# Kernel tuning notes

Measured on AMD Instinct MI355X. Metric: run time of the kernel, lower is better.

## Reference

```python
import jax, jax.numpy as jnp
import numpy as np

VOCAB, E, H, P, B, S = 30522, 1024, 1024, 16, 32, 256
HD = H // 2  # per-direction LSTM hidden


def _lstm_dir(xt, Wih, Whh, bih, bhh, reverse):
    # xt: [S,B,in]; PyTorch gate order i,f,g,o
    Hd = Whh.shape[1]
    Bz = xt.shape[1]
    bias = bih + bhh

    def step(carry, xb):
        h, c = carry
        g = xb @ Wih.T + h @ Whh.T + bias
        i, f, gg, o = jnp.split(g, 4, axis=-1)
        c = jax.nn.sigmoid(f) * c + jax.nn.sigmoid(i) * jnp.tanh(gg)
        h = jax.nn.sigmoid(o) * jnp.tanh(c)
        return (h, c), h

    init = (jnp.zeros((Bz, Hd), xt.dtype), jnp.zeros((Bz, Hd), xt.dtype))
    _, hs = jax.lax.scan(step, init, xt, reverse=reverse)
    return hs  # [S,B,Hd], time-ordered


def _bilstm(x, Wih, Whh, bih, bhh):
    # x: [B,S,in]; Wih: [2,4*HD,in] (dir 0 = fwd, dir 1 = bwd)
    xt = jnp.swapaxes(x, 0, 1)
    fw = _lstm_dir(xt, Wih[0], Whh[0], bih[0], bhh[0], False)
    bw = _lstm_dir(xt, Wih[1], Whh[1], bih[1], bhh[1], True)
    return jnp.swapaxes(jnp.concatenate([fw, bw], axis=-1), 0, 1)  # [B,S,2*HD]


def setup_inputs() -> dict:
    key = jax.random.key(0)
    ks = jax.random.split(key, 20)
    sc = 0.05
    inp = {}
    inp["emb"] = jax.random.normal(ks[0], (VOCAB, E), jnp.float32) * sc
    inp["ctx_emb"] = jax.random.normal(ks[1], (VOCAB, E), jnp.float32) * sc
    inp["prompt_emb"] = jax.random.normal(ks[2], (P, E), jnp.float32) * sc
    # LSTM layer 0: input E; layer 1: input 2*HD = H
    inp["Wih0"] = jax.random.normal(ks[3], (2, 4 * HD, E), jnp.float32) * sc
    inp["Whh0"] = jax.random.normal(ks[4], (2, 4 * HD, HD), jnp.float32) * sc
    inp["bih0"] = jax.random.normal(ks[5], (2, 4 * HD), jnp.float32) * sc
    inp["bhh0"] = jax.random.normal(ks[6], (2, 4 * HD), jnp.float32) * sc
    inp["Wih1"] = jax.random.normal(ks[7], (2, 4 * HD, H), jnp.float32) * sc
    inp["Whh1"] = jax.random.normal(ks[8], (2, 4 * HD, HD), jnp.float32) * sc
    inp["bih1"] = jax.random.normal(ks[9], (2, 4 * HD), jnp.float32) * sc
    inp["bhh1"] = jax.random.normal(ks[10], (2, 4 * HD), jnp.float32) * sc
    inp["W1"] = jax.random.normal(ks[11], (H, H), jnp.float32) * sc
    inp["b1"] = jnp.zeros((H,), jnp.float32)
    inp["W2"] = jax.random.normal(ks[12], (E, H), jnp.float32) * sc
    inp["b2"] = jnp.zeros((E,), jnp.float32)
    inp["input_ids"] = jax.random.randint(ks[13], (B, S), 0, VOCAB)
    # distinct, sorted prompt positions per batch row (torch loop assumes valid slots)
    pk = jax.random.split(ks[14], B)
    perms = jax.vmap(lambda k: jax.random.permutation(k, S)[:P])(pk)
    inp["prompt_indexes"] = jnp.sort(perms, axis=1)
    return inp


def reference(emb, ctx_emb, prompt_emb, Wih0, Whh0, bih0, bhh0,
              Wih1, Whh1, bih1, bhh1, W1, b1, W2, b2,
              input_ids, prompt_indexes):
    raw = emb[input_ids]                               # [B,S,E]
    b_idx = jnp.arange(input_ids.shape[0])[:, None]    # [B,1]
    # unique_prompt branch: detached raw + ctx embedding, scatter prompt embeds
    allb = jax.lax.stop_gradient(raw) + ctx_emb[input_ids]
    allb = allb.at[b_idx, prompt_indexes].set(
        jnp.broadcast_to(prompt_emb, (input_ids.shape[0],) + prompt_emb.shape))
    h = _bilstm(allb, Wih0, Whh0, bih0, bhh0)
    h = _bilstm(h, Wih1, Whh1, bih1, bhh1)             # [B,S,H]
    out = jax.nn.relu(h @ W1.T + b1) @ W2.T + b2       # [B,S,E]
    upd = out[b_idx, prompt_indexes] + prompt_emb      # [B,P,E]
    return raw.at[b_idx, prompt_indexes].set(upd)
```

## Files before the change

kernel.cpp:

```cpp
#include <hip/hip_runtime.h>
#include <hip/hip_bf16.h>
#include <math.h>

constexpr int NB  = 32;
constexpr int NS  = 256;
constexpr int NE  = 1024;
constexpr int NH  = 1024;
constexpr int NHD = 512;
constexpr int NG  = 2048;
constexpr int NP  = 16;
constexpr int NBS = NB * NS;
constexpr int GK  = 1024;

constexpr int UPW  = 16;
constexpr int NWGD = NHD / UPW;
constexpr size_t GT_DIR = (size_t)NWGD * 256 * 2048;

typedef __attribute__((ext_vector_type(8))) short bf16x8;
typedef __attribute__((ext_vector_type(4))) float f32x4;
typedef unsigned short u16;

__device__ __forceinline__ float sigm(float x) { return 1.0f / (1.0f + __expf(-x)); }
__device__ __forceinline__ u16 f2bf(float f) {
    union { float f; unsigned u; } v; v.f = f;
    unsigned r = v.u + 0x7FFF + ((v.u >> 16) & 1);
    return (u16)(r >> 16);
}
__device__ __forceinline__ float bf2f(u16 b) {
    return __uint_as_float((unsigned)b << 16);
}

__global__ void k_zero(int* p) { p[threadIdx.x] = 0; }

__global__ void k_allb(const float* __restrict__ emb, const float* __restrict__ ctx,
                       const float* __restrict__ pemb, const int* __restrict__ ids,
                       const int* __restrict__ pidx, u16* __restrict__ allb) {
    int r = blockIdx.x;
    int b = r >> 8, s = r & 255;
    __shared__ int ppos;
    if (threadIdx.x == 0) {
        int t = -1;
        #pragma unroll
        for (int p = 0; p < NP; ++p)
            if (pidx[b * NP + p] == s) t = p;
        ppos = t;
    }
    __syncthreads();
    int e = threadIdx.x;
    float4 v;
    if (ppos >= 0) {
        v = ((const float4*)(pemb + (size_t)ppos * NE))[e];
    } else {
        int id = ids[r];
        float4 a = ((const float4*)(emb + (size_t)id * NE))[e];
        float4 c = ((const float4*)(ctx + (size_t)id * NE))[e];
        v = make_float4(a.x + c.x, a.y + c.y, a.z + c.z, a.w + c.w);
    }
    ushort4 o;
    o.x = f2bf(v.x); o.y = f2bf(v.y); o.z = f2bf(v.z); o.w = f2bf(v.w);
    *(ushort4*)(allb + ((size_t)(s * NB + b)) * NE + e * 4) = o;
}

__global__ void k_raw(const float* __restrict__ emb, const int* __restrict__ ids,
                      float* __restrict__ out) {
    int r = blockIdx.x;
    int id = ids[r];
    ((float4*)(out + (size_t)r * NE))[threadIdx.x] =
        ((const float4*)(emb + (size_t)id * NE))[threadIdx.x];
}

__global__ void k_wcvt(const float* __restrict__ Wih, const float* __restrict__ bih,
                       const float* __restrict__ bhh, u16* __restrict__ Wbf,
                       float* __restrict__ biasC) {
    int blk = blockIdx.x;
    int d = blk >> 11, np = blk & 2047;
    int rw = (np & 3) * 512 + (np >> 2);
    const float* src = Wih + ((size_t)d * NG + rw) * GK;
    u16* dst = Wbf + ((size_t)d * NG + np) * GK;
    int t = threadIdx.x;
    float4 v = ((const float4*)src)[t];
    ushort4 o;
    o.x = f2bf(v.x); o.y = f2bf(v.y); o.z = f2bf(v.z); o.w = f2bf(v.w);
    ((ushort4*)dst)[t] = o;
    if (t == 0)
        biasC[d * NG + np] = bih[d * NG + rw] + bhh[d * NG + rw];
}

__global__ __launch_bounds__(256) void k_gemm_m(const u16* __restrict__ A0,
                                                const u16* __restrict__ A1,
                                                int astride,
                                                const u16* __restrict__ W,
                                                const float* __restrict__ bc,
                                                float* __restrict__ Gt) {
    __shared__ char At[128 * 128];
    __shared__ char Wt[128 * 128];
    int tid = threadIdx.x;
    int lane = tid & 63, w = tid >> 6;
    int n0 = blockIdx.x * 128, m0 = blockIdx.y * 128;
    int r = tid >> 1, h = tid & 1;

    f32x4 acc[4][4];
    #pragma unroll
    for (int i = 0; i < 4; ++i)
        #pragma unroll
        for (int j = 0; j < 4; ++j) acc[i][j] = (f32x4){0.f, 0.f, 0.f, 0.f};

    unsigned rsw = (unsigned)((r & 7) << 4);
    for (int kt = 0; kt < GK; kt += 64) {
        {
            int k0 = kt + h * 32;
            const u16* asrc = (k0 < 512) ? (A0 + (size_t)(m0 + r) * astride + k0)
                                         : (A1 + (size_t)(m0 + r) * astride + (k0 - 512));
            const u16* wsrc = W + (size_t)(n0 + r) * GK + k0;
            #pragma unroll
            for (int j = 0; j < 4; ++j) {
                uint4 va = *(const uint4*)(asrc + j * 8);
                *(uint4*)(At + r * 128 + (((unsigned)(h * 64 + j * 16)) ^ rsw)) = va;
                uint4 vw = *(const uint4*)(wsrc + j * 8);
                *(uint4*)(Wt + r * 128 + (((unsigned)(h * 64 + j * 16)) ^ rsw)) = vw;
            }
        }
        __syncthreads();
        #pragma unroll
        for (int sub = 0; sub < 2; ++sub) {
            bf16x8 af[4], bfr[4];
            int kbyte = sub * 64 + (lane >> 4) * 16;
            #pragma unroll
            for (int ni = 0; ni < 4; ++ni) {
                int rr = (w & 1) * 64 + ni * 16 + (lane & 15);
                af[ni] = *(const bf16x8*)(Wt + rr * 128 + ((unsigned)kbyte ^ ((unsigned)((rr & 7) << 4))));
            }
            #pragma unroll
            for (int mi = 0; mi < 4; ++mi) {
                int rr = (w >> 1) * 64 + mi * 16 + (lane & 15);
                bfr[mi] = *(const bf16x8*)(At + rr * 128 + ((unsigned)kbyte ^ ((unsigned)((rr & 7) << 4))));
            }
            #pragma unroll
            for (int mi = 0; mi < 4; ++mi)
                #pragma unroll
                for (int ni = 0; ni < 4; ++ni)
                    acc[mi][ni] = __builtin_amdgcn_mfma_f32_16x16x32_bf16(
                        af[ni], bfr[mi], acc[mi][ni], 0, 0, 0);
        }
        __syncthreads();
    }
    #pragma unroll
    for (int mi = 0; mi < 4; ++mi) {
        int mp = m0 + (w >> 1) * 64 + mi * 16 + (lane & 15);
        int t = mp >> 5, b = mp & 31;
        #pragma unroll
        for (int ni = 0; ni < 4; ++ni) {
            int npb = n0 + (w & 1) * 64 + ni * 16 + (lane >> 4) * 4;
            int unit = npb >> 2;
            float4 bv = *(const float4*)(bc + npb);
            f32x4 a = acc[mi][ni];
            float4 o = make_float4(a[0] + bv.x, a[1] + bv.y, a[2] + bv.z, a[3] + bv.w);
            *(float4*)(Gt + ((size_t)((unit >> 4) * NS + t)) * 2048 + b * 64 + (unit & 15) * 4) = o;
        }
    }
}

__global__ __launch_bounds__(256) void k_lstm_s(const float* __restrict__ Gt,
                                                const float* __restrict__ Whh,
                                                u16* __restrict__ hxb,
                                                int* __restrict__ ctr) {
    __shared__ char hlds[NB * NHD * 2];
    int wg = blockIdx.x;
    int d = wg & 1;
    int slice = wg >> 1;
    int n0 = slice * UPW;
    int tid = threadIdx.x;
    int lane = tid & 63;
    int w = tid >> 6;
    int* ctrd  = ctr + d * 64;
    int* myctr = ctrd + (slice & 3) * 16;
    u16* hxd = hxb + (size_t)d * NS * NB * NHD;
    const float* Gd = Gt + (size_t)d * GT_DIR + (size_t)slice * NS * 2048;

    bf16x8 wfrag[16];
    {
        int rloc = lane & 15;
        int usub = rloc >> 2, g = rloc & 3;
        int kb = lane >> 4;
        const float* wrow = Whh + ((size_t)d * NG + g * NHD + n0 + 4 * w + usub) * NHD;
        #pragma unroll
        for (int kk = 0; kk < 16; ++kk) {
            const float* p = wrow + kk * 32 + kb * 8;
            float4 x = *(const float4*)p;
            float4 y = *(const float4*)(p + 4);
            bf16x8 wf;
            wf[0] = (short)f2bf(x.x); wf[1] = (short)f2bf(x.y);
            wf[2] = (short)f2bf(x.z); wf[3] = (short)f2bf(x.w);
            wf[4] = (short)f2bf(y.x); wf[5] = (short)f2bf(y.y);
            wf[6] = (short)f2bf(y.z); wf[7] = (short)f2bf(y.w);
            wfrag[kk] = wf;
        }
    }
    int uloc  = 4 * w + (lane >> 4);
    int unitC = n0 + uloc;
    int bcol0 = lane & 15;
    int bcol1 = 16 + bcol0;
    int kb    = lane >> 4;
    int c8 = tid & 7, bRow = tid >> 3;

    float c0 = 0.f, c1 = 0.f;
    int ttp = d ? (NS - 1) : 0;
    float4 Gv0 = *(const float4*)(Gd + (size_t)ttp * 2048 + bcol0 * 64 + uloc * 4);
    float4 Gv1 = *(const float4*)(Gd + (size_t)ttp * 2048 + bcol1 * 64 + uloc * 4);

    for (int step = 0; step < NS; ++step) {
        int tt = d ? (NS - 1 - step) : step;
        f32x4 acc0 = {0.f, 0.f, 0.f, 0.f};
        f32x4 acc1 = {0.f, 0.f, 0.f, 0.f};
        if (step) {
            int tprev = d ? tt + 1 : tt - 1;
            const u16* srow = hxd + ((size_t)tprev * NB + bRow) * NHD;
            char* dstrow = hlds + bRow * 1024;
            unsigned rsw = (unsigned)((bRow & 7) << 4);
            #pragma unroll
            for (int i = 0; i < 8; ++i) {
                uint4 v = *(const uint4*)(srow + c8 * 64 + i * 8);
                *(uint4*)(dstrow + (((unsigned)(c8 * 128 + i * 16)) ^ rsw)) = v;
            }
            __syncthreads();
            const char* b0base = hlds + bcol0 * 1024;
            const char* b1base = hlds + bcol1 * 1024;
            unsigned s0 = (unsigned)((bcol0 & 7) << 4);
            unsigned s1 = (unsigned)((bcol1 & 7) << 4);
            #pragma unroll
            for (int kk = 0; kk < 16; ++kk) {
                bf16x8 b0 = *(const bf16x8*)(b0base + (((unsigned)(kk * 64 + kb * 16)) ^ s0));
                bf16x8 b1 = *(const bf16x8*)(b1base + (((unsigned)(kk * 64 + kb * 16)) ^ s1));
                acc0 = __builtin_amdgcn_mfma_f32_16x16x32_bf16(wfrag[kk], b0, acc0, 0, 0, 0);
                acc1 = __builtin_amdgcn_mfma_f32_16x16x32_bf16(wfrag[kk], b1, acc1, 0, 0, 0);
            }
        }
        {
            float ig = sigm(acc0[0] + Gv0.x);
            float fg = sigm(acc0[1] + Gv0.y);
            float gg = tanhf(acc0[2] + Gv0.z);
            float og = sigm(acc0[3] + Gv0.w);
            c0 = fg * c0 + ig * gg;
            float hv = og * tanhf(c0);
            __hip_atomic_store(hxd + ((size_t)tt * NB + bcol0) * NHD + unitC, f2bf(hv),
                               __ATOMIC_RELAXED, __HIP_MEMORY_SCOPE_AGENT);
        }
        {
            float ig = sigm(acc1[0] + Gv1.x);
            float fg = sigm(acc1[1] + Gv1.y);
            float gg = tanhf(acc1[2] + Gv1.z);
            float og = sigm(acc1[3] + Gv1.w);
            c1 = fg * c1 + ig * gg;
            float hv = og * tanhf(c1);
            __hip_atomic_store(hxd + ((size_t)tt * NB + bcol1) * NHD + unitC, f2bf(hv),
                               __ATOMIC_RELAXED, __HIP_MEMORY_SCOPE_AGENT);
        }
        asm volatile("s_waitcnt vmcnt(0)" ::: "memory");
        __syncthreads();
        if (tid == 0)
            __hip_atomic_fetch_add(myctr, 1, __ATOMIC_RELAXED, __HIP_MEMORY_SCOPE_AGENT);
        if (step + 1 < NS) {
            int ttn = d ? tt - 1 : tt + 1;
            Gv0 = *(const float4*)(Gd + (size_t)ttn * 2048 + bcol0 * 64 + uloc * 4);
            Gv1 = *(const float4*)(Gd + (size_t)ttn * 2048 + bcol1 * 64 + uloc * 4);
        }
        asm volatile("" ::: "memory");
        if (tid == 0) {
            int target = (NWGD / 4) * (step + 1);
            for (;;) {
                int a = __hip_atomic_load(ctrd +  0, __ATOMIC_RELAXED, __HIP_MEMORY_SCOPE_AGENT);
                int b = __hip_atomic_load(ctrd + 16, __ATOMIC_RELAXED, __HIP_MEMORY_SCOPE_AGENT);
                int c = __hip_atomic_load(ctrd + 32, __ATOMIC_RELAXED, __HIP_MEMORY_SCOPE_AGENT);
                int e = __hip_atomic_load(ctrd + 48, __ATOMIC_RELAXED, __HIP_MEMORY_SCOPE_AGENT);
                if (a >= target && b >= target && c >= target && e >= target) break;
                __builtin_amdgcn_s_sleep(1);
            }
        }
        __syncthreads();
    }
}

__global__ __launch_bounds__(256) void k_mlp1(const u16* __restrict__ hxb,
                                              const int* __restrict__ pidx,
                                              const float* __restrict__ W1,
                                              const float* __restrict__ b1,
                                              float* __restrict__ mid) {
    __shared__ float As[16][65];
    __shared__ float Ws[16][65];
    int tid = threadIdx.x;
    int tx = tid & 15, ty = tid >> 4;
    int n0 = blockIdx.x * 64, m0 = blockIdx.y * 64;
    int lr = tid >> 2;
    int lk = (tid & 3) * 4;
    int m = m0 + lr;
    int bb = m >> 4;
    int s = pidx[m];
    float acc[4][4] = {};
    for (int kt = 0; kt < GK; kt += 16) {
        int k0 = kt + lk;
        int half = k0 >> 9;
        ushort4 av4 = *(const ushort4*)(hxb + (((size_t)(half * NS + s)) * NB + bb) * NHD + (k0 & 511));
        float4 wv = *(const float4*)(W1 + (size_t)(n0 + lr) * GK + k0);
        As[lk + 0][lr] = bf2f(av4.x); As[lk + 1][lr] = bf2f(av4.y);
        As[lk + 2][lr] = bf2f(av4.z); As[lk + 3][lr] = bf2f(av4.w);
        Ws[lk + 0][lr] = wv.x; Ws[lk + 1][lr] = wv.y;
        Ws[lk + 2][lr] = wv.z; Ws[lk + 3][lr] = wv.w;
        __syncthreads();
        #pragma unroll
        for (int kk = 0; kk < 16; ++kk) {
            float a[4], wv2[4];
            #pragma unroll
            for (int i = 0; i < 4; ++i) a[i] = As[kk][ty * 4 + i];
            #pragma unroll
            for (int j = 0; j < 4; ++j) wv2[j] = Ws[kk][tx * 4 + j];
            #pragma unroll
            for (int i = 0; i < 4; ++i)
                #pragma unroll
                for (int j = 0; j < 4; ++j) acc[i][j] += a[i] * wv2[j];
        }
        __syncthreads();
    }
    #pragma unroll
    for (int j = 0; j < 4; ++j) {
        int n = n0 + tx * 4 + j;
        float bias = b1[n];
        #pragma unroll
        for (int i = 0; i < 4; ++i)
            mid[(size_t)(m0 + ty * 4 + i) * 1024 + n] = fmaxf(acc[i][j] + bias, 0.f);
    }
}

__global__ __launch_bounds__(256) void k_mlp2(const float* __restrict__ mid,
                                              const int* __restrict__ pidx,
                                              const float* __restrict__ W2,
                                              const float* __restrict__ b2,
                                              const float* __restrict__ pemb,
                                              float* __restrict__ out) {
    __shared__ float As[16][65];
    __shared__ float Ws[16][65];
    int tid = threadIdx.x;
    int tx = tid & 15, ty = tid >> 4;
    int n0 = blockIdx.x * 64, m0 = blockIdx.y * 64;
    int lr = tid >> 2;
    int lk = (tid & 3) * 4;
    float acc[4][4] = {};
    for (int kt = 0; kt < GK; kt += 16) {
        float4 av = *(const float4*)(mid + (size_t)(m0 + lr) * GK + kt + lk);
        float4 wv = *(const float4*)(W2 + (size_t)(n0 + lr) * GK + kt + lk);
        As[lk + 0][lr] = av.x; As[lk + 1][lr] = av.y;
        As[lk + 2][lr] = av.z; As[lk + 3][lr] = av.w;
        Ws[lk + 0][lr] = wv.x; Ws[lk + 1][lr] = wv.y;
        Ws[lk + 2][lr] = wv.z; Ws[lk + 3][lr] = wv.w;
        __syncthreads();
        #pragma unroll
        for (int kk = 0; kk < 16; ++kk) {
            float a[4], wv2[4];
            #pragma unroll
            for (int i = 0; i < 4; ++i) a[i] = As[kk][ty * 4 + i];
            #pragma unroll
            for (int j = 0; j < 4; ++j) wv2[j] = Ws[kk][tx * 4 + j];
            #pragma unroll
            for (int i = 0; i < 4; ++i)
                #pragma unroll
                for (int j = 0; j < 4; ++j) acc[i][j] += a[i] * wv2[j];
        }
        __syncthreads();
    }
    #pragma unroll
    for (int i = 0; i < 4; ++i) {
        int m = m0 + ty * 4 + i;
        int bb = m >> 4, p = m & 15;
        int s = pidx[m];
        float* orow = out + ((size_t)(bb * NS + s)) * NE;
        const float* prow = pemb + (size_t)p * NE;
        #pragma unroll
        for (int j = 0; j < 4; ++j) {
            int n = n0 + tx * 4 + j;
            orow[n] = acc[i][j] + b2[n] + prow[n];
        }
    }
}

extern "C" void kernel_launch(void* const* d_in, const int* in_sizes, int n_in,
                              void* d_out, int out_size, void* d_ws, size_t ws_size,
                              hipStream_t stream) {
    const float* emb  = (const float*)d_in[0];
    const float* ctx  = (const float*)d_in[1];
    const float* pemb = (const float*)d_in[2];
    const float* Wih0 = (const float*)d_in[3];
    const float* Whh0 = (const float*)d_in[4];
    const float* bih0 = (const float*)d_in[5];
    const float* bhh0 = (const float*)d_in[6];
    const float* Wih1 = (const float*)d_in[7];
    const float* Whh1 = (const float*)d_in[8];
    const float* bih1 = (const float*)d_in[9];
    const float* bhh1 = (const float*)d_in[10];
    const float* W1   = (const float*)d_in[11];
    const float* b1   = (const float*)d_in[12];
    const float* W2   = (const float*)d_in[13];
    const float* b2   = (const float*)d_in[14];
    const int* ids    = (const int*)d_in[15];
    const int* pidx   = (const int*)d_in[16];
    float* out = (float*)d_out;

    char* ws = (char*)d_ws;
    float* Gt    = (float*)ws;
    u16*   allb  = (u16*)(ws + 134217728u);
    u16*   hx    = (u16*)(ws + 150994944u);
    u16*   Wbf   = (u16*)(ws + 167772160u);
    float* biasC = (float*)(ws + 176160768u);
    float* mid   = (float*)(ws + 176177152u);
    int*   ctr   = (int*)(ws + 178274304u);

    k_zero<<<dim3(1), dim3(256), 0, stream>>>(ctr);
    k_allb<<<dim3(NBS), dim3(256), 0, stream>>>(emb, ctx, pemb, ids, pidx, allb);

    k_wcvt<<<dim3(2 * NG), dim3(256), 0, stream>>>(Wih0, bih0, bhh0, Wbf, biasC);
    for (int d = 0; d < 2; ++d)
        k_gemm_m<<<dim3(NG / 128, NBS / 128), dim3(256), 0, stream>>>(
            allb, allb + 512, 1024, Wbf + (size_t)d * NG * GK, biasC + d * NG,
            Gt + (size_t)d * GT_DIR);
    k_lstm_s<<<dim3(2 * NWGD), dim3(256), 0, stream>>>(Gt, Whh0, hx, ctr);

    k_raw<<<dim3(NBS), dim3(256), 0, stream>>>(emb, ids, out);

    k_wcvt<<<dim3(2 * NG), dim3(256), 0, stream>>>(Wih1, bih1, bhh1, Wbf, biasC);
    for (int d = 0; d < 2; ++d)
        k_gemm_m<<<dim3(NG / 128, NBS / 128), dim3(256), 0, stream>>>(
            hx, hx + (size_t)NS * NB * NHD, 512, Wbf + (size_t)d * NG * GK,
            biasC + d * NG, Gt + (size_t)d * GT_DIR);
    k_lstm_s<<<dim3(2 * NWGD), dim3(256), 0, stream>>>(Gt, Whh1, hx, ctr + 128);

    k_mlp1<<<dim3(16, 8), dim3(256), 0, stream>>>(hx, pidx, W1, b1, mid);
    k_mlp2<<<dim3(16, 8), dim3(256), 0, stream>>>(mid, pidx, W2, b2, pemb, out);
}
```

Baseline: 2.418 ms.

## Replace atomic counter barrier with per-workgroup flag lines polled by whole wavefronts

The grid-wide barrier in the persistent LSTM kernel no longer has every workgroup atomically increment one of four shared counters. Each workgroup now stores its step number to its own cache line, and every wave polls all 32 workgroup flags in parallel with a wave-wide vote. This removes atomic contention, the single-thread spin and the trailing __syncthreads, and skips the barrier after the last step. The cost is more polling traffic and a larger counter area that must be zeroed, now done by 8 blocks.

```diff
diff --git a/kernel.cpp b/kernel.cpp
--- a/kernel.cpp
+++ b/kernel.cpp
@@ -30,7 +30,7 @@
     return __uint_as_float((unsigned)b << 16);
 }
 
-__global__ void k_zero(int* p) { p[threadIdx.x] = 0; }
+__global__ void k_zero(int* p) { p[blockIdx.x * 256 + threadIdx.x] = 0; }
 
 __global__ void k_allb(const float* __restrict__ emb, const float* __restrict__ ctx,
                        const float* __restrict__ pemb, const int* __restrict__ ids,
@@ -160,10 +160,10 @@
     }
 }
 
-__global__ __launch_bounds__(256) void k_lstm_s(const float* __restrict__ Gt,
+__global__ __launch_bounds__(256) void k_lstm_p(const float* __restrict__ Gt,
                                                 const float* __restrict__ Whh,
                                                 u16* __restrict__ hxb,
-                                                int* __restrict__ ctr) {
+                                                int* __restrict__ cblk) {
     __shared__ char hlds[NB * NHD * 2];
     int wg = blockIdx.x;
     int d = wg & 1;
@@ -172,8 +172,9 @@
     int tid = threadIdx.x;
     int lane = tid & 63;
     int w = tid >> 6;
-    int* ctrd  = ctr + d * 64;
-    int* myctr = ctrd + (slice & 3) * 16;
+    int* lines  = cblk + d * 512;
+    int* myline = lines + slice * 16;
+    int pollidx = (lane & 31) * 16;
     u16* hxd = hxb + (size_t)d * NS * NB * NHD;
     const float* Gd = Gt + (size_t)d * GT_DIR + (size_t)slice * NS * 2048;
 
@@ -255,28 +256,27 @@
             __hip_atomic_store(hxd + ((size_t)tt * NB + bcol1) * NHD + unitC, f2bf(hv),
                                __ATOMIC_RELAXED, __HIP_MEMORY_SCOPE_AGENT);
         }
+        if (step == NS - 1) break;
         asm volatile("s_waitcnt vmcnt(0)" ::: "memory");
         __syncthreads();
         if (tid == 0)
-            __hip_atomic_fetch_add(myctr, 1, __ATOMIC_RELAXED, __HIP_MEMORY_SCOPE_AGENT);
-        if (step + 1 < NS) {
+            __hip_atomic_store(myline, step + 1, __ATOMIC_RELAXED,
+                               __HIP_MEMORY_SCOPE_AGENT);
+        {
             int ttn = d ? tt - 1 : tt + 1;
             Gv0 = *(const float4*)(Gd + (size_t)ttn * 2048 + bcol0 * 64 + uloc * 4);
             Gv1 = *(const float4*)(Gd + (size_t)ttn * 2048 + bcol1 * 64 + uloc * 4);
         }
         asm volatile("" ::: "memory");
-        if (tid == 0) {
-            int target = (NWGD / 4) * (step + 1);
+        {
+            int target = step + 1;
             for (;;) {
-                int a = __hip_atomic_load(ctrd +  0, __ATOMIC_RELAXED, __HIP_MEMORY_SCOPE_AGENT);
-                int b = __hip_atomic_load(ctrd + 16, __ATOMIC_RELAXED, __HIP_MEMORY_SCOPE_AGENT);
-                int c = __hip_atomic_load(ctrd + 32, __ATOMIC_RELAXED, __HIP_MEMORY_SCOPE_AGENT);
-                int e = __hip_atomic_load(ctrd + 48, __ATOMIC_RELAXED, __HIP_MEMORY_SCOPE_AGENT);
-                if (a >= target && b >= target && c >= target && e >= target) break;
+                int v = __hip_atomic_load(lines + pollidx, __ATOMIC_RELAXED,
+                                          __HIP_MEMORY_SCOPE_AGENT);
+                if (__all(v >= target)) break;
                 __builtin_amdgcn_s_sleep(1);
             }
         }
-        __syncthreads();
     }
 }
 
@@ -412,7 +412,7 @@
     float* mid   = (float*)(ws + 176177152u);
     int*   ctr   = (int*)(ws + 178274304u);
 
-    k_zero<<<dim3(1), dim3(256), 0, stream>>>(ctr);
+    k_zero<<<dim3(8), dim3(256), 0, stream>>>(ctr);
     k_allb<<<dim3(NBS), dim3(256), 0, stream>>>(emb, ctx, pemb, ids, pidx, allb);
 
     k_wcvt<<<dim3(2 * NG), dim3(256), 0, stream>>>(Wih0, bih0, bhh0, Wbf, biasC);
@@ -420,7 +420,7 @@
         k_gemm_m<<<dim3(NG / 128, NBS / 128), dim3(256), 0, stream>>>(
             allb, allb + 512, 1024, Wbf + (size_t)d * NG * GK, biasC + d * NG,
             Gt + (size_t)d * GT_DIR);
-    k_lstm_s<<<dim3(2 * NWGD), dim3(256), 0, stream>>>(Gt, Whh0, hx, ctr);
+    k_lstm_p<<<dim3(2 * NWGD), dim3(256), 0, stream>>>(Gt, Whh0, hx, ctr);
 
     k_raw<<<dim3(NBS), dim3(256), 0, stream>>>(emb, ids, out);
 
@@ -429,7 +429,7 @@
         k_gemm_m<<<dim3(NG / 128, NBS / 128), dim3(256), 0, stream>>>(
             hx, hx + (size_t)NS * NB * NHD, 512, Wbf + (size_t)d * NG * GK,
             biasC + d * NG, Gt + (size_t)d * GT_DIR);
-    k_lstm_s<<<dim3(2 * NWGD), dim3(256), 0, stream>>>(Gt, Whh1, hx, ctr + 128);
+    k_lstm_p<<<dim3(2 * NWGD), dim3(256), 0, stream>>>(Gt, Whh1, hx, ctr + 1024);
 
     k_mlp1<<<dim3(16, 8), dim3(256), 0, stream>>>(hx, pidx, W1, b1, mid);
     k_mlp2<<<dim3(16, 8), dim3(256), 0, stream>>>(mid, pidx, W2, b2, pemb, out);
```

Result: faster. 2.363 ms (-2.3%).
